# Optimization experiments

Hardware: AMD Instinct MI355X
Metric: run time of the kernel (lower is better)

Reference implementation:

```python
import jax, jax.numpy as jnp
import numpy as np

D_MODEL = 256
N_HEADS = 8
B, S = 8, 2048
TEMP = jnp.sqrt(jnp.float32(D_MODEL))  # ScaledDotProductAttention(temperature=d_model) -> sqrt(d_model)
NEG = jnp.float32(-1e9)


def setup_inputs() -> dict:
    key = jax.random.key(0)
    ks = jax.random.split(key, 12)
    dh = D_MODEL * N_HEADS
    sc_in = 1.0 / np.sqrt(D_MODEL)
    sc_out = 1.0 / np.sqrt(dh)
    return {
        "query": jax.random.normal(ks[0], (B, S, D_MODEL), jnp.float32),
        "key": jax.random.normal(ks[1], (B, S, D_MODEL), jnp.float32),
        "value": jax.random.normal(ks[2], (B, S, D_MODEL), jnp.float32),
        "mask": jax.random.bernoulli(ks[3], 0.9, (B, S)),
        "Wq": jax.random.normal(ks[4], (D_MODEL, dh), jnp.float32) * sc_in,
        "bq": jnp.zeros((dh,), jnp.float32),
        "Wk": jax.random.normal(ks[5], (D_MODEL, dh), jnp.float32) * sc_in,
        "bk": jnp.zeros((dh,), jnp.float32),
        "Wv": jax.random.normal(ks[6], (D_MODEL, dh), jnp.float32) * sc_in,
        "bv": jnp.zeros((dh,), jnp.float32),
        "Wo": jax.random.normal(ks[7], (dh, D_MODEL), jnp.float32) * sc_out,
        "bo": jnp.zeros((D_MODEL,), jnp.float32),
    }


def reference(query, key, value, mask, Wq, bq, Wk, bk, Wv, bv, Wo, bo):
    nb = query.shape[0]
    # projections: (B,S,d) @ (d, d*H) -> view (B,S,H,d)
    q = (query @ Wq + bq).reshape(nb, -1, N_HEADS, D_MODEL)
    k = (key @ Wk + bk).reshape(nb, -1, N_HEADS, D_MODEL)
    v = (value @ Wv + bv).reshape(nb, -1, N_HEADS, D_MODEL)
    # torch.matmul on (B,S,H,d): batched over (B,S) -> per-position HxH attention
    attn = jnp.einsum('bshd,bsgd->bshg', q, k) / TEMP
    m = mask[:, :, None, None]  # (B,S,1,1) broadcast, as in mask.view(B,-1,1,1)
    attn = jnp.where(m, attn, NEG)
    attn = jax.nn.softmax(attn, axis=-1)  # dropout p=0 -> identity
    x = jnp.einsum('bshg,bsgd->bshd', attn, v)  # (B,S,H,d)
    # x.transpose(1,2).contiguous().view(B,-1,d*H)
    x = jnp.transpose(x, (0, 2, 1, 3)).reshape(nb, -1, D_MODEL * N_HEADS)
    return x @ Wo + bo
```

## Files before the change

### kernel.cpp

```cpp
#include <hip/hip_runtime.h>
#include <hip/hip_bf16.h>

typedef __hip_bfloat16 bf16;
typedef short bf16x8 __attribute__((ext_vector_type(8)));
typedef float f32x4 __attribute__((ext_vector_type(4)));

#define MFMA16(a,b,c) __builtin_amdgcn_mfma_f32_16x16x32_bf16(a,b,c,0,0,0)

__device__ __forceinline__ unsigned short f2us(float x){
    union{__hip_bfloat16 h; unsigned short u;} c; c.h = __float2bfloat16(x); return c.u;
}
__device__ __forceinline__ float us2f(unsigned short u){
    union{unsigned short u; __hip_bfloat16 h;} c; c.u = u; return __bfloat162float(c.h);
}
__device__ __forceinline__ uint4 pack8(float4 a, float4 b){
    union{unsigned short us[8]; uint4 v;} p;
    p.us[0]=f2us(a.x); p.us[1]=f2us(a.y); p.us[2]=f2us(a.z); p.us[3]=f2us(a.w);
    p.us[4]=f2us(b.x); p.us[5]=f2us(b.y); p.us[6]=f2us(b.z); p.us[7]=f2us(b.w);
    return p.v;
}

__global__ __launch_bounds__(256) void prep_kernel(
    const float* __restrict__ Wq, const float* __restrict__ Wk,
    const float* __restrict__ Wv, const float* __restrict__ bq,
    const float* __restrict__ bk, const float* __restrict__ bv,
    const float* __restrict__ Wo,
    bf16* __restrict__ WqT, bf16* __restrict__ WkT, bf16* __restrict__ WvT,
    float* __restrict__ bqp, float* __restrict__ bkp, float* __restrict__ bvp,
    bf16* __restrict__ WoT)
{
    __shared__ float T[64][68];
    const int tid = threadIdx.x, bx = blockIdx.x;
    if (bx < 384) {
        const int mat = bx / 128, rem = bx % 128;
        const int c0 = (rem >> 5) * 64, n0 = (rem & 31) * 64;
        const float* W = (mat == 0) ? Wq : (mat == 1) ? Wk : Wv;
        bf16* WT = (mat == 0) ? WqT : (mat == 1) ? WkT : WvT;
        #pragma unroll
        for (int it = 0; it < 4; ++it) {
            int pp = tid + (it << 8);
            int cl = pp >> 4, n4 = (pp & 15) * 4;
            float4 f = *(const float4*)(W + (size_t)(c0 + cl) * 2048 + n0 + n4);
            T[cl][n4] = f.x; T[cl][n4+1] = f.y; T[cl][n4+2] = f.z; T[cl][n4+3] = f.w;
        }
        __syncthreads();
        const int h = n0 >> 8, d0 = n0 & 255;
        #pragma unroll
        for (int it = 0; it < 2; ++it) {
            int pp = tid + (it << 8);
            int j = pp >> 3, g = pp & 7;
            union{unsigned short us[8]; uint4 v;} pk;
            #pragma unroll
            for (int u = 0; u < 8; ++u) pk.us[u] = f2us(T[g*8+u][j]);
            *(uint4*)(WT + (size_t)((d0 + j) * 8 + h) * 256 + c0 + g * 8) = pk.v;
        }
    } else if (bx < 387) {
        const int mat = bx - 384;
        const float* src = (mat == 0) ? bq : (mat == 1) ? bk : bv;
        float* dst = (mat == 0) ? bqp : (mat == 1) ? bkp : bvp;
        for (int n = tid; n < 2048; n += 256)
            dst[(n & 255) * 8 + (n >> 8)] = src[n];
    } else {
        const int idx = bx - 387;
        const int k0 = (idx >> 2) * 64, c0 = (idx & 3) * 64;
        #pragma unroll
        for (int it = 0; it < 4; ++it) {
            int pp = tid + (it << 8);
            int kl = pp >> 4, c4 = (pp & 15) * 4;
            float4 f = *(const float4*)(Wo + (size_t)(k0 + kl) * 256 + c0 + c4);
            T[kl][c4] = f.x; T[kl][c4+1] = f.y; T[kl][c4+2] = f.z; T[kl][c4+3] = f.w;
        }
        __syncthreads();
        #pragma unroll
        for (int it = 0; it < 2; ++it) {
            int pp = tid + (it << 8);
            int j = pp >> 3, g = pp & 7;
            union{unsigned short us[8]; uint4 v;} pk;
            #pragma unroll
            for (int u = 0; u < 8; ++u) pk.us[u] = f2us(T[g*8+u][j]);
            *(uint4*)(WoT + (size_t)(c0 + j) * 2048 + k0 + g * 8) = pk.v;
        }
    }
}

__global__ __launch_bounds__(512) void qk_kernel(
    const float* __restrict__ Qin, const float* __restrict__ Kin,
    const int* __restrict__ mask,
    const bf16* __restrict__ WqT, const bf16* __restrict__ WkT,
    const float* __restrict__ bqp, const float* __restrict__ bkp,
    float* __restrict__ w)
{
    __shared__ __align__(16) char smem[147456];
    char* const Xq = smem;
    char* const Xk = smem + 32768;
    char* const QT = smem + 65536;
    char* const KT = smem + 106496;
    float* const RED = (float*)smem;

    const int tid  = threadIdx.x;
    const int wid  = tid >> 6, lane = tid & 63;
    const int quad = lane >> 4, l15 = lane & 15;
    const int tok0 = blockIdx.x * 64;

    #pragma unroll
    for (int it = 0; it < 4; ++it) {
        int pp = tid + (it << 9);
        int row = pp >> 5, g = pp & 31;
        const float* s = Qin + (size_t)(tok0 + row) * 256 + g * 8;
        *(uint4*)(Xq + row * 512 + ((g ^ (row & 7)) << 4)) =
            pack8(*(const float4*)s, *(const float4*)(s + 4));
        s = Kin + (size_t)(tok0 + row) * 256 + g * 8;
        *(uint4*)(Xk + row * 512 + ((g ^ (row & 7)) << 4)) =
            pack8(*(const float4*)s, *(const float4*)(s + 4));
    }
    __syncthreads();

    f32x4 sacc[4];
    #pragma unroll
    for (int p = 0; p < 4; ++p)
        #pragma unroll
        for (int i = 0; i < 4; ++i) sacc[p][i] = 0.f;

    const int pll = wid * 16 + l15;

    for (int Cp = 0; Cp < 8; ++Cp) {
        #pragma unroll
        for (int par = 0; par < 2; ++par) {
            const int C = Cp * 2 + par;
            f32x4 accq[4], acck[4];
            #pragma unroll
            for (int mt = 0; mt < 4; ++mt)
                #pragma unroll
                for (int i = 0; i < 4; ++i) { accq[mt][i] = 0.f; acck[mt][i] = 0.f; }
            #pragma unroll
            for (int Ks = 0; Ks < 8; ++Ks) {
                bf16x8 bq = *(const bf16x8*)(WqT + (size_t)(C * 128 + pll) * 256 + Ks * 32 + quad * 8);
                bf16x8 bk = *(const bf16x8*)(WkT + (size_t)(C * 128 + pll) * 256 + Ks * 32 + quad * 8);
                #pragma unroll
                for (int mt = 0; mt < 4; ++mt) {
                    int row = mt * 16 + l15;
                    int G = (Ks * 4 + quad) ^ (row & 7);
                    bf16x8 a = *(const bf16x8*)(Xq + row * 512 + (G << 4));
                    accq[mt] = MFMA16(a, bq, accq[mt]);
                    a = *(const bf16x8*)(Xk + row * 512 + (G << 4));
                    acck[mt] = MFMA16(a, bk, acck[mt]);
                }
            }
            const int p2 = par * 128 + pll;
            const int rowoff = p2 * 160 + ((p2 >> 6) & 3) * 8;
            const float biq = bqp[C * 128 + pll];
            const float bik = bkp[C * 128 + pll];
            #pragma unroll
            for (int mt = 0; mt < 4; ++mt) {
                int t0 = mt * 16 + quad * 4;
                union{unsigned short us[4]; uint2 v;} pq, pk;
                #pragma unroll
                for (int i = 0; i < 4; ++i) {
                    pq.us[i] = f2us(accq[mt][i] + biq);
                    pk.us[i] = f2us(acck[mt][i] + bik);
                }
                *(uint2*)(QT + rowoff + t0 * 2) = pq.v;
                *(uint2*)(KT + rowoff + t0 * 2) = pk.v;
            }
        }
        __syncthreads();
        #pragma unroll
        for (int pp2 = 0; pp2 < 4; ++pp2) {
            int tq = 2 * (wid * 4 + pp2) + (l15 >> 3);
            union{unsigned short us[8]; bf16x8 v;} Aq, Bk;
            #pragma unroll
            for (int j = 0; j < 8; ++j) {
                int p2 = (quad * 8 + j) * 8 + (l15 & 7);
                int off = p2 * 160 + ((p2 >> 6) & 3) * 8 + tq * 2;
                Aq.us[j] = *(const unsigned short*)(QT + off);
                Bk.us[j] = *(const unsigned short*)(KT + off);
            }
            sacc[pp2] = MFMA16(Aq.v, Bk.v, sacc[pp2]);
        }
        __syncthreads();
    }

    if ((quad >> 1) == (l15 >> 3)) {
        #pragma unroll
        for (int pp2 = 0; pp2 < 4; ++pp2) {
            int tl = (wid * 4 + pp2) * 2 + (l15 >> 3);
            #pragma unroll
            for (int i = 0; i < 4; ++i)
                RED[tl * 68 + ((quad & 1) * 4 + i) * 8 + (l15 & 7)] = sacc[pp2][i];
        }
    }
    __syncthreads();
    {
        const int tl = tid >> 3, hh = tid & 7;
        const int mk = mask[tok0 + tl];
        const float* r = RED + tl * 68 + hh * 8;
        float m = r[0];
        #pragma unroll
        for (int g = 1; g < 8; ++g) m = fmaxf(m, r[g]);
        float e[8], sum = 0.f;
        #pragma unroll
        for (int g = 0; g < 8; ++g) { e[g] = __expf((r[g] - m) * 0.0625f); sum += e[g]; }
        float inv = 1.f / sum;
        float o[8];
        #pragma unroll
        for (int g = 0; g < 8; ++g) o[g] = mk ? e[g] * inv : 0.125f;
        float* wp = w + (size_t)(tok0 + tl) * 64 + hh * 8;
        *(float4*)wp = make_float4(o[0], o[1], o[2], o[3]);
        *(float4*)(wp + 4) = make_float4(o[4], o[5], o[6], o[7]);
    }
}

__global__ __launch_bounds__(512) void v_attn_kernel(
    const float* __restrict__ Vin,
    const bf16* __restrict__ WvT, const float* __restrict__ bvp,
    const float* __restrict__ w, bf16* __restrict__ A)
{
    __shared__ __align__(16) char smem[66560];
    char* const Xv = smem;
    char* const VT = smem + 32768;
    char* const xS = smem + 50176;

    const int tid  = threadIdx.x;
    const int wid  = tid >> 6, lane = tid & 63;
    const int quad = lane >> 4, l15 = lane & 15;
    const int tok0 = blockIdx.x * 64;
    const int t6   = tid & 63, dg = tid >> 6;

    #pragma unroll
    for (int it = 0; it < 4; ++it) {
        int pp = tid + (it << 9);
        int row = pp >> 5, g = pp & 31;
        const float* s = Vin + (size_t)(tok0 + row) * 256 + g * 8;
        *(uint4*)(Xv + row * 512 + ((g ^ (row & 7)) << 4)) =
            pack8(*(const float4*)s, *(const float4*)(s + 4));
    }
    float wv[64];
    {
        const float* wp = w + (size_t)(tok0 + t6) * 64;
        #pragma unroll
        for (int i = 0; i < 16; ++i) {
            float4 f = ((const float4*)wp)[i];
            wv[i*4] = f.x; wv[i*4+1] = f.y; wv[i*4+2] = f.z; wv[i*4+3] = f.w;
        }
    }
    __syncthreads();

    const int pll = wid * 16 + l15;

    for (int C = 0; C < 16; ++C) {
        f32x4 acc[4];
        #pragma unroll
        for (int mt = 0; mt < 4; ++mt)
            #pragma unroll
            for (int i = 0; i < 4; ++i) acc[mt][i] = 0.f;
        #pragma unroll
        for (int Ks = 0; Ks < 8; ++Ks) {
            bf16x8 b = *(const bf16x8*)(WvT + (size_t)(C * 128 + pll) * 256 + Ks * 32 + quad * 8);
            #pragma unroll
            for (int mt = 0; mt < 4; ++mt) {
                int row = mt * 16 + l15;
                int G = (Ks * 4 + quad) ^ (row & 7);
                bf16x8 a = *(const bf16x8*)(Xv + row * 512 + (G << 4));
                acc[mt] = MFMA16(a, b, acc[mt]);
            }
        }
        const float biv = bvp[C * 128 + pll];
        #pragma unroll
        for (int mt = 0; mt < 4; ++mt) {
            int t0 = mt * 16 + quad * 4;
            union{unsigned short us[4]; uint2 v;} pk;
            #pragma unroll
            for (int i = 0; i < 4; ++i) pk.us[i] = f2us(acc[mt][i] + biv);
            *(uint2*)(VT + pll * 136 + t0 * 2) = pk.v;
        }
        __syncthreads();
        #pragma unroll
        for (int dd = 0; dd < 2; ++dd) {
            int d = dg * 2 + dd;
            float vv[8];
            #pragma unroll
            for (int g = 0; g < 8; ++g)
                vv[g] = us2f(*(const unsigned short*)(VT + (d * 8 + g) * 136 + t6 * 2));
            #pragma unroll
            for (int h = 0; h < 8; ++h) {
                float x = 0.f;
                #pragma unroll
                for (int g = 0; g < 8; ++g) x = fmaf(wv[h * 8 + g], vv[g], x);
                int u = (h * 2 + (d >> 3)) ^ (t6 & 15);
                *(unsigned short*)(xS + t6 * 256 + u * 16 + (d & 7) * 2) = f2us(x);
            }
        }
        __syncthreads();
        {
            int t = tid >> 3, hh = tid & 7;
            int tok = tok0 + t;
            int b = tok >> 11, sr = tok & 2047, sg = sr >> 3, j = sr & 7;
            size_t r = ((size_t)b << 11) + hh * 256 + sg;
            bf16* dst = A + r * 2048 + j * 256 + C * 16;
            int u0 = (hh * 2) ^ (t & 15), u1 = (hh * 2 + 1) ^ (t & 15);
            *(uint4*)dst       = *(const uint4*)(xS + t * 256 + u0 * 16);
            *(uint4*)(dst + 8) = *(const uint4*)(xS + t * 256 + u1 * 16);
        }
    }
}

__global__ __launch_bounds__(256) void outproj_kernel(
    const bf16* __restrict__ A, const bf16* __restrict__ WoT,
    const float* __restrict__ Wo, const float* __restrict__ bo,
    float* __restrict__ Out)
{
    __shared__ __align__(16) char smem[24576];
    char* const AsS = smem;
    char* const Ws  = smem + 8192;

    const int tid = threadIdx.x;
    const int wave = tid >> 6, lane = tid & 63, quad = lane >> 4, l15 = lane & 15;
    const int R = blockIdx.x >> 1, C = blockIdx.x & 1;
    const int row0 = R * 64, col0 = C * 128;

    f32x4 acc[4][2];
    #pragma unroll
    for (int mt = 0; mt < 4; ++mt)
        #pragma unroll
        for (int nt = 0; nt < 2; ++nt)
            #pragma unroll
            for (int i = 0; i < 4; ++i) acc[mt][nt][i] = 0.f;

    for (int kc = 0; kc < 32; ++kc) {
        __syncthreads();
        #pragma unroll
        for (int it = 0; it < 2; ++it) {
            int pp = tid + (it << 8);
            int rho = pp >> 3, g = pp & 7;
            *(uint4*)(AsS + rho * 128 + ((g ^ (rho & 7)) << 4)) =
                *(const uint4*)(A + (size_t)(row0 + rho) * 2048 + kc * 64 + g * 8);
        }
        if (WoT != nullptr) {
            #pragma unroll
            for (int it = 0; it < 4; ++it) {
                int pp = tid + (it << 8);
                int cl = pp >> 3, g = pp & 7;
                *(uint4*)(Ws + cl * 128 + ((g ^ (cl & 7)) << 4)) =
                    *(const uint4*)(WoT + (size_t)(col0 + cl) * 2048 + kc * 64 + g * 8);
            }
        } else {
            #pragma unroll
            for (int it = 0; it < 8; ++it) {
                int pp = tid + (it << 8);
                int kl = pp >> 5, c4 = (pp & 31) * 4;
                float4 f = *(const float4*)(Wo + (size_t)(kc * 64 + kl) * 256 + col0 + c4);
                float fv[4] = {f.x, f.y, f.z, f.w};
                #pragma unroll
                for (int u = 0; u < 4; ++u) {
                    int cl = c4 + u;
                    *(unsigned short*)(Ws + cl * 128 + (((kl >> 3) ^ (cl & 7)) << 4) + (kl & 7) * 2)
                        = f2us(fv[u]);
                }
            }
        }
        __syncthreads();
        #pragma unroll
        for (int ks = 0; ks < 2; ++ks) {
            bf16x8 a[4], b[2];
            #pragma unroll
            for (int mt = 0; mt < 4; ++mt) {
                int row = mt * 16 + l15;
                int G = (ks * 4 + quad) ^ (row & 7);
                a[mt] = *(const bf16x8*)(AsS + row * 128 + (G << 4));
            }
            #pragma unroll
            for (int nt = 0; nt < 2; ++nt) {
                int cl = wave * 32 + nt * 16 + l15;
                int G = (ks * 4 + quad) ^ (cl & 7);
                b[nt] = *(const bf16x8*)(Ws + cl * 128 + (G << 4));
            }
            #pragma unroll
            for (int mt = 0; mt < 4; ++mt)
                #pragma unroll
                for (int nt = 0; nt < 2; ++nt)
                    acc[mt][nt] = MFMA16(a[mt], b[nt], acc[mt][nt]);
        }
    }
    #pragma unroll
    for (int nt = 0; nt < 2; ++nt) {
        int col = col0 + wave * 32 + nt * 16 + l15;
        float bias = bo[col];
        #pragma unroll
        for (int mt = 0; mt < 4; ++mt) {
            int r0 = row0 + mt * 16 + quad * 4;
            #pragma unroll
            for (int i = 0; i < 4; ++i)
                Out[(size_t)(r0 + i) * 256 + col] = acc[mt][nt][i] + bias;
        }
    }
}

extern "C" void kernel_launch(void* const* d_in, const int* in_sizes, int n_in,
                              void* d_out, int out_size, void* d_ws, size_t ws_size,
                              hipStream_t stream) {
    const float* query = (const float*)d_in[0];
    const float* key   = (const float*)d_in[1];
    const float* value = (const float*)d_in[2];
    const int*   mask  = (const int*)  d_in[3];
    const float* Wq = (const float*)d_in[4];  const float* bq = (const float*)d_in[5];
    const float* Wk = (const float*)d_in[6];  const float* bk = (const float*)d_in[7];
    const float* Wv = (const float*)d_in[8];  const float* bv = (const float*)d_in[9];
    const float* Wo = (const float*)d_in[10]; const float* bo = (const float*)d_in[11];

    char* dc = (char*)d_out;
    bf16*  WqT = (bf16*)dc;
    bf16*  WkT = (bf16*)(dc + 1048576);
    bf16*  WvT = (bf16*)(dc + 2097152);
    float* bqp = (float*)(dc + 3145728);
    float* bkp = (float*)(dc + 3153920);
    float* bvp = (float*)(dc + 3162112);
    float* w   = (float*)(dc + 3170304);

    bf16* A = (bf16*)d_ws;
    const bool big = ws_size >= (67108864ull + 1048576ull);
    bf16* WoT = big ? (bf16*)((char*)d_ws + 67108864) : nullptr;

    prep_kernel<<<big ? 515 : 387, 256, 0, stream>>>(
        Wq, Wk, Wv, bq, bk, bv, Wo, WqT, WkT, WvT, bqp, bkp, bvp, WoT);
    qk_kernel<<<256, 512, 0, stream>>>(
        query, key, mask, WqT, WkT, bqp, bkp, w);
    v_attn_kernel<<<256, 512, 0, stream>>>(value, WvT, bvp, w, A);
    outproj_kernel<<<512, 256, 0, stream>>>(A, WoT, Wo, bo, (float*)d_out);
}
```

Baseline: 305.7 us.

## Restructure QK/V projection tiles with swapped MFMA operands and bf16 attention weights

The Wq/Wk weight and bias layouts are permuted so each 256-wide chunk groups heads contiguously. The qk and v kernels swap MFMA operands so weights are the A operand, with two M-tiles per wave. Results are staged in a padded, swizzled token-major LDS layout, which lets the per-token QK^T MFMA read vectorized 16-byte fragments instead of scalar gathers. Attention weights are stored as bf16 instead of fp32, and the v kernel writes its output directly without the extra xS staging pass and barrier. The intent is to cut LDS gather cost, barriers and global traffic, at the cost of lower precision in the attention weights and different launch-bounds occupancy hints.

```diff
diff --git a/kernel.cpp b/kernel.cpp
--- a/kernel.cpp
+++ b/kernel.cpp
@@ -52,14 +52,21 @@
             union{unsigned short us[8]; uint4 v;} pk;
             #pragma unroll
             for (int u = 0; u < 8; ++u) pk.us[u] = f2us(T[g*8+u][j]);
-            *(uint4*)(WT + (size_t)((d0 + j) * 8 + h) * 256 + c0 + g * 8) = pk.v;
+            int d = d0 + j;
+            size_t row;
+            if (mat < 2) row = (size_t)((d >> 5) * 256 + h * 32 + (d & 31));
+            else         row = (size_t)(d * 8 + h);
+            *(uint4*)(WT + row * 256 + c0 + g * 8) = pk.v;
         }
     } else if (bx < 387) {
         const int mat = bx - 384;
         const float* src = (mat == 0) ? bq : (mat == 1) ? bk : bv;
         float* dst = (mat == 0) ? bqp : (mat == 1) ? bkp : bvp;
-        for (int n = tid; n < 2048; n += 256)
-            dst[(n & 255) * 8 + (n >> 8)] = src[n];
+        for (int n = tid; n < 2048; n += 256) {
+            int h = n >> 8, d = n & 255;
+            int idx = (mat < 2) ? ((d >> 5) * 256 + h * 32 + (d & 31)) : (d * 8 + h);
+            dst[idx] = src[n];
+        }
     } else {
         const int idx = bx - 387;
         const int k0 = (idx >> 2) * 64, c0 = (idx & 3) * 64;
@@ -83,22 +90,22 @@
     }
 }
 
-__global__ __launch_bounds__(512) void qk_kernel(
+__global__ __launch_bounds__(512, 2) void qk_kernel(
     const float* __restrict__ Qin, const float* __restrict__ Kin,
     const int* __restrict__ mask,
-    const bf16* __restrict__ WqT, const bf16* __restrict__ WkT,
-    const float* __restrict__ bqp, const float* __restrict__ bkp,
-    float* __restrict__ w)
+    const bf16* __restrict__ WqTs, const bf16* __restrict__ WkTs,
+    const float* __restrict__ bqs, const float* __restrict__ bks,
+    bf16* __restrict__ wbf)
 {
-    __shared__ __align__(16) char smem[147456];
+    __shared__ __align__(16) char smem[133120];
     char* const Xq = smem;
     char* const Xk = smem + 32768;
     char* const QT = smem + 65536;
-    char* const KT = smem + 106496;
+    char* const KT = smem + 99328;
     float* const RED = (float*)smem;
 
     const int tid  = threadIdx.x;
-    const int wid  = tid >> 6, lane = tid & 63;
+    const int wave = tid >> 6, lane = tid & 63;
     const int quad = lane >> 4, l15 = lane & 15;
     const int tok0 = blockIdx.x * 64;
 
@@ -121,72 +128,76 @@
         #pragma unroll
         for (int i = 0; i < 4; ++i) sacc[p][i] = 0.f;
 
-    const int pll = wid * 16 + l15;
-
-    for (int Cp = 0; Cp < 8; ++Cp) {
-        #pragma unroll
-        for (int par = 0; par < 2; ++par) {
-            const int C = Cp * 2 + par;
-            f32x4 accq[4], acck[4];
-            #pragma unroll
-            for (int mt = 0; mt < 4; ++mt)
-                #pragma unroll
-                for (int i = 0; i < 4; ++i) { accq[mt][i] = 0.f; acck[mt][i] = 0.f; }
+    for (int W = 0; W < 8; ++W) {
+        #pragma unroll
+        for (int mat = 0; mat < 2; ++mat) {
+            const bf16* WT = mat ? WkTs : WqTs;
+            const char* Xb = mat ? Xk : Xq;
+            const float* bs = mat ? bks : bqs;
+            char* RT = mat ? KT : QT;
+            f32x4 acc[2][4];
+            #pragma unroll
+            for (int m = 0; m < 2; ++m)
+                #pragma unroll
+                for (int nt = 0; nt < 4; ++nt)
+                    #pragma unroll
+                    for (int i = 0; i < 4; ++i) acc[m][nt][i] = 0.f;
             #pragma unroll
             for (int Ks = 0; Ks < 8; ++Ks) {
-                bf16x8 bq = *(const bf16x8*)(WqT + (size_t)(C * 128 + pll) * 256 + Ks * 32 + quad * 8);
-                bf16x8 bk = *(const bf16x8*)(WkT + (size_t)(C * 128 + pll) * 256 + Ks * 32 + quad * 8);
-                #pragma unroll
-                for (int mt = 0; mt < 4; ++mt) {
-                    int row = mt * 16 + l15;
-                    int G = (Ks * 4 + quad) ^ (row & 7);
-                    bf16x8 a = *(const bf16x8*)(Xq + row * 512 + (G << 4));
-                    accq[mt] = MFMA16(a, bq, accq[mt]);
-                    a = *(const bf16x8*)(Xk + row * 512 + (G << 4));
-                    acck[mt] = MFMA16(a, bk, acck[mt]);
+                bf16x8 af[2];
+                #pragma unroll
+                for (int m = 0; m < 2; ++m)
+                    af[m] = *(const bf16x8*)(WT +
+                        (size_t)(W * 256 + (wave * 2 + m) * 16 + l15) * 256 + Ks * 32 + quad * 8);
+                #pragma unroll
+                for (int nt = 0; nt < 4; ++nt) {
+                    int tok = nt * 16 + l15;
+                    int G = (Ks * 4 + quad) ^ (tok & 7);
+                    bf16x8 bfv = *(const bf16x8*)(Xb + tok * 512 + (G << 4));
+                    #pragma unroll
+                    for (int m = 0; m < 2; ++m)
+                        acc[m][nt] = MFMA16(af[m], bfv, acc[m][nt]);
                 }
             }
-            const int p2 = par * 128 + pll;
-            const int rowoff = p2 * 160 + ((p2 >> 6) & 3) * 8;
-            const float biq = bqp[C * 128 + pll];
-            const float bik = bkp[C * 128 + pll];
-            #pragma unroll
-            for (int mt = 0; mt < 4; ++mt) {
-                int t0 = mt * 16 + quad * 4;
-                union{unsigned short us[4]; uint2 v;} pq, pk;
-                #pragma unroll
-                for (int i = 0; i < 4; ++i) {
-                    pq.us[i] = f2us(accq[mt][i] + biq);
-                    pk.us[i] = f2us(acck[mt][i] + bik);
+            #pragma unroll
+            for (int m = 0; m < 2; ++m) {
+                int Sb = (wave * 2 + m) * 16 + quad * 4;
+                float4 b4 = *(const float4*)(bs + W * 256 + Sb);
+                int u = (wave * 2 + m) * 2 + (quad >> 1);
+                #pragma unroll
+                for (int nt = 0; nt < 4; ++nt) {
+                    int tok = nt * 16 + l15;
+                    int up = (u & 24) | ((u + 2 * tok) & 7);
+                    union{unsigned short us[4]; uint2 v;} pk;
+                    pk.us[0] = f2us(acc[m][nt][0] + b4.x);
+                    pk.us[1] = f2us(acc[m][nt][1] + b4.y);
+                    pk.us[2] = f2us(acc[m][nt][2] + b4.z);
+                    pk.us[3] = f2us(acc[m][nt][3] + b4.w);
+                    *(uint2*)(RT + tok * 528 + up * 16 + (quad & 1) * 8) = pk.v;
                 }
-                *(uint2*)(QT + rowoff + t0 * 2) = pq.v;
-                *(uint2*)(KT + rowoff + t0 * 2) = pk.v;
-            }
-        }
-        __syncthreads();
-        #pragma unroll
-        for (int pp2 = 0; pp2 < 4; ++pp2) {
-            int tq = 2 * (wid * 4 + pp2) + (l15 >> 3);
-            union{unsigned short us[8]; bf16x8 v;} Aq, Bk;
-            #pragma unroll
-            for (int j = 0; j < 8; ++j) {
-                int p2 = (quad * 8 + j) * 8 + (l15 & 7);
-                int off = p2 * 160 + ((p2 >> 6) & 3) * 8 + tq * 2;
-                Aq.us[j] = *(const unsigned short*)(QT + off);
-                Bk.us[j] = *(const unsigned short*)(KT + off);
-            }
-            sacc[pp2] = MFMA16(Aq.v, Bk.v, sacc[pp2]);
+            }
+        }
+        __syncthreads();
+        #pragma unroll
+        for (int pp = 0; pp < 4; ++pp) {
+            int tok = (wave * 4 + pp) * 2 + (l15 >> 3);
+            int h = l15 & 7;
+            int u = h * 4 + quad;
+            int up = (u & 24) | ((u + 2 * tok) & 7);
+            bf16x8 Aq = *(const bf16x8*)(QT + tok * 528 + up * 16);
+            bf16x8 Bk = *(const bf16x8*)(KT + tok * 528 + up * 16);
+            sacc[pp] = MFMA16(Aq, Bk, sacc[pp]);
         }
         __syncthreads();
     }
 
     if ((quad >> 1) == (l15 >> 3)) {
         #pragma unroll
-        for (int pp2 = 0; pp2 < 4; ++pp2) {
-            int tl = (wid * 4 + pp2) * 2 + (l15 >> 3);
+        for (int pp = 0; pp < 4; ++pp) {
+            int tl = (wave * 4 + pp) * 2 + (l15 >> 3);
             #pragma unroll
             for (int i = 0; i < 4; ++i)
-                RED[tl * 68 + ((quad & 1) * 4 + i) * 8 + (l15 & 7)] = sacc[pp2][i];
+                RED[tl * 68 + ((quad & 1) * 4 + i) * 8 + (l15 & 7)] = sacc[pp][i];
         }
     }
     __syncthreads();
@@ -201,30 +212,27 @@
         #pragma unroll
         for (int g = 0; g < 8; ++g) { e[g] = __expf((r[g] - m) * 0.0625f); sum += e[g]; }
         float inv = 1.f / sum;
-        float o[8];
-        #pragma unroll
-        for (int g = 0; g < 8; ++g) o[g] = mk ? e[g] * inv : 0.125f;
-        float* wp = w + (size_t)(tok0 + tl) * 64 + hh * 8;
-        *(float4*)wp = make_float4(o[0], o[1], o[2], o[3]);
-        *(float4*)(wp + 4) = make_float4(o[4], o[5], o[6], o[7]);
-    }
-}
-
-__global__ __launch_bounds__(512) void v_attn_kernel(
+        union{unsigned short us[8]; uint4 v;} pk;
+        #pragma unroll
+        for (int g = 0; g < 8; ++g) pk.us[g] = f2us(mk ? e[g] * inv : 0.125f);
+        *(uint4*)(wbf + (size_t)(tok0 + tl) * 64 + hh * 8) = pk.v;
+    }
+}
+
+__global__ __launch_bounds__(512, 4) void v_attn_kernel(
     const float* __restrict__ Vin,
     const bf16* __restrict__ WvT, const float* __restrict__ bvp,
-    const float* __restrict__ w, bf16* __restrict__ A)
+    const bf16* __restrict__ wbf, bf16* __restrict__ A)
 {
     __shared__ __align__(16) char smem[66560];
     char* const Xv = smem;
     char* const VT = smem + 32768;
-    char* const xS = smem + 50176;
 
     const int tid  = threadIdx.x;
-    const int wid  = tid >> 6, lane = tid & 63;
+    const int wave = tid >> 6, lane = tid & 63;
     const int quad = lane >> 4, l15 = lane & 15;
     const int tok0 = blockIdx.x * 64;
-    const int t6   = tid & 63, dg = tid >> 6;
+    const int t6 = tid & 63, dg = tid >> 6;
 
     #pragma unroll
     for (int it = 0; it < 4; ++it) {
@@ -234,73 +242,93 @@
         *(uint4*)(Xv + row * 512 + ((g ^ (row & 7)) << 4)) =
             pack8(*(const float4*)s, *(const float4*)(s + 4));
     }
-    float wv[64];
+    unsigned wvp[32];
     {
-        const float* wp = w + (size_t)(tok0 + t6) * 64;
-        #pragma unroll
-        for (int i = 0; i < 16; ++i) {
-            float4 f = ((const float4*)wp)[i];
-            wv[i*4] = f.x; wv[i*4+1] = f.y; wv[i*4+2] = f.z; wv[i*4+3] = f.w;
+        const uint4* wp = (const uint4*)(wbf + (size_t)(tok0 + t6) * 64);
+        #pragma unroll
+        for (int i = 0; i < 8; ++i) {
+            uint4 v = wp[i];
+            wvp[i*4] = v.x; wvp[i*4+1] = v.y; wvp[i*4+2] = v.z; wvp[i*4+3] = v.w;
         }
     }
     __syncthreads();
 
-    const int pll = wid * 16 + l15;
-
-    for (int C = 0; C < 16; ++C) {
-        f32x4 acc[4];
-        #pragma unroll
-        for (int mt = 0; mt < 4; ++mt)
-            #pragma unroll
-            for (int i = 0; i < 4; ++i) acc[mt][i] = 0.f;
+    const int gtok = tok0 + t6;
+    const int bb = gtok >> 11, sr = gtok & 2047, sg = sr >> 3, jj = sr & 7;
+
+    for (int W = 0; W < 8; ++W) {
+        f32x4 acc[2][4];
+        #pragma unroll
+        for (int m = 0; m < 2; ++m)
+            #pragma unroll
+            for (int nt = 0; nt < 4; ++nt)
+                #pragma unroll
+                for (int i = 0; i < 4; ++i) acc[m][nt][i] = 0.f;
         #pragma unroll
         for (int Ks = 0; Ks < 8; ++Ks) {
-            bf16x8 b = *(const bf16x8*)(WvT + (size_t)(C * 128 + pll) * 256 + Ks * 32 + quad * 8);
-            #pragma unroll
-            for (int mt = 0; mt < 4; ++mt) {
-                int row = mt * 16 + l15;
-                int G = (Ks * 4 + quad) ^ (row & 7);
-                bf16x8 a = *(const bf16x8*)(Xv + row * 512 + (G << 4));
-                acc[mt] = MFMA16(a, b, acc[mt]);
-            }
-        }
-        const float biv = bvp[C * 128 + pll];
-        #pragma unroll
-        for (int mt = 0; mt < 4; ++mt) {
-            int t0 = mt * 16 + quad * 4;
+            bf16x8 af[2];
+            #pragma unroll
+            for (int m = 0; m < 2; ++m)
+                af[m] = *(const bf16x8*)(WvT +
+                    (size_t)(W * 256 + (wave * 2 + m) * 16 + l15) * 256 + Ks * 32 + quad * 8);
+            #pragma unroll
+            for (int nt = 0; nt < 4; ++nt) {
+                int tok = nt * 16 + l15;
+                int G = (Ks * 4 + quad) ^ (tok & 7);
+                bf16x8 bfv = *(const bf16x8*)(Xv + tok * 512 + (G << 4));
+                #pragma unroll
+                for (int m = 0; m < 2; ++m)
+                    acc[m][nt] = MFMA16(af[m], bfv, acc[m][nt]);
+            }
+        }
+        #pragma unroll
+        for (int m = 0; m < 2; ++m) {
+            int Sb = (wave * 2 + m) * 16 + quad * 4;
+            float4 b4 = *(const float4*)(bvp + W * 256 + Sb);
+            int u = (wave * 2 + m) * 2 + (quad >> 1);
+            #pragma unroll
+            for (int nt = 0; nt < 4; ++nt) {
+                int tok = nt * 16 + l15;
+                int up = (u & 24) | ((u + 2 * tok) & 7);
+                union{unsigned short us[4]; uint2 v;} pk;
+                pk.us[0] = f2us(acc[m][nt][0] + b4.x);
+                pk.us[1] = f2us(acc[m][nt][1] + b4.y);
+                pk.us[2] = f2us(acc[m][nt][2] + b4.z);
+                pk.us[3] = f2us(acc[m][nt][3] + b4.w);
+                *(uint2*)(VT + tok * 528 + up * 16 + (quad & 1) * 8) = pk.v;
+            }
+        }
+        __syncthreads();
+        float vvf[4][8];
+        #pragma unroll
+        for (int dd = 0; dd < 4; ++dd) {
+            int u = dg * 4 + dd;
+            int up = (u & 24) | ((u + 2 * t6) & 7);
+            bf16x8 v8 = *(const bf16x8*)(VT + t6 * 528 + up * 16);
+            #pragma unroll
+            for (int g = 0; g < 8; ++g) vvf[dd][g] = us2f((unsigned short)v8[g]);
+        }
+        #pragma unroll
+        for (int h = 0; h < 8; ++h) {
+            float wf[8];
+            #pragma unroll
+            for (int g2 = 0; g2 < 4; ++g2) {
+                unsigned u2 = wvp[h * 4 + g2];
+                wf[g2*2]   = us2f((unsigned short)(u2 & 0xffff));
+                wf[g2*2+1] = us2f((unsigned short)(u2 >> 16));
+            }
             union{unsigned short us[4]; uint2 v;} pk;
             #pragma unroll
-            for (int i = 0; i < 4; ++i) pk.us[i] = f2us(acc[mt][i] + biv);
-            *(uint2*)(VT + pll * 136 + t0 * 2) = pk.v;
-        }
-        __syncthreads();
-        #pragma unroll
-        for (int dd = 0; dd < 2; ++dd) {
-            int d = dg * 2 + dd;
-            float vv[8];
-            #pragma unroll
-            for (int g = 0; g < 8; ++g)
-                vv[g] = us2f(*(const unsigned short*)(VT + (d * 8 + g) * 136 + t6 * 2));
-            #pragma unroll
-            for (int h = 0; h < 8; ++h) {
+            for (int dd = 0; dd < 4; ++dd) {
                 float x = 0.f;
                 #pragma unroll
-                for (int g = 0; g < 8; ++g) x = fmaf(wv[h * 8 + g], vv[g], x);
-                int u = (h * 2 + (d >> 3)) ^ (t6 & 15);
-                *(unsigned short*)(xS + t6 * 256 + u * 16 + (d & 7) * 2) = f2us(x);
-            }
-        }
-        __syncthreads();
-        {
-            int t = tid >> 3, hh = tid & 7;
-            int tok = tok0 + t;
-            int b = tok >> 11, sr = tok & 2047, sg = sr >> 3, j = sr & 7;
-            size_t r = ((size_t)b << 11) + hh * 256 + sg;
-            bf16* dst = A + r * 2048 + j * 256 + C * 16;
-            int u0 = (hh * 2) ^ (t & 15), u1 = (hh * 2 + 1) ^ (t & 15);
-            *(uint4*)dst       = *(const uint4*)(xS + t * 256 + u0 * 16);
-            *(uint4*)(dst + 8) = *(const uint4*)(xS + t * 256 + u1 * 16);
-        }
+                for (int g = 0; g < 8; ++g) x = fmaf(wf[g], vvf[dd][g], x);
+                pk.us[dd] = f2us(x);
+            }
+            size_t r = ((size_t)bb << 11) + h * 256 + sg;
+            *(uint2*)(A + r * 2048 + jj * 256 + W * 32 + dg * 4) = pk.v;
+        }
+        __syncthreads();
     }
 }
 
@@ -408,22 +436,22 @@
     const float* Wo = (const float*)d_in[10]; const float* bo = (const float*)d_in[11];
 
     char* dc = (char*)d_out;
-    bf16*  WqT = (bf16*)dc;
-    bf16*  WkT = (bf16*)(dc + 1048576);
-    bf16*  WvT = (bf16*)(dc + 2097152);
-    float* bqp = (float*)(dc + 3145728);
-    float* bkp = (float*)(dc + 3153920);
-    float* bvp = (float*)(dc + 3162112);
-    float* w   = (float*)(dc + 3170304);
+    bf16*  WqTs = (bf16*)dc;
+    bf16*  WkTs = (bf16*)(dc + 1048576);
+    bf16*  WvT  = (bf16*)(dc + 2097152);
+    float* bqs  = (float*)(dc + 3145728);
+    float* bks  = (float*)(dc + 3153920);
+    float* bvp  = (float*)(dc + 3162112);
+    bf16*  wbf  = (bf16*)(dc + 3170304);
 
     bf16* A = (bf16*)d_ws;
     const bool big = ws_size >= (67108864ull + 1048576ull);
     bf16* WoT = big ? (bf16*)((char*)d_ws + 67108864) : nullptr;
 
     prep_kernel<<<big ? 515 : 387, 256, 0, stream>>>(
-        Wq, Wk, Wv, bq, bk, bv, Wo, WqT, WkT, WvT, bqp, bkp, bvp, WoT);
+        Wq, Wk, Wv, bq, bk, bv, Wo, WqTs, WkTs, WvT, bqs, bks, bvp, WoT);
     qk_kernel<<<256, 512, 0, stream>>>(
-        query, key, mask, WqT, WkT, bqp, bkp, w);
-    v_attn_kernel<<<256, 512, 0, stream>>>(value, WvT, bvp, w, A);
+        query, key, mask, WqTs, WkTs, bqs, bks, wbf);
+    v_attn_kernel<<<256, 512, 0, stream>>>(value, WvT, bvp, wbf, A);
     outproj_kernel<<<512, 256, 0, stream>>>(A, WoT, Wo, bo, (float*)d_out);
 }
```

Measured after the change: 498.4 us. 63.0% more time.
